# Kernel optimization log

Measured on AMD Instinct MI355X. Metric: run time of the kernel, lower is better.

## Reference

```python
import jax, jax.numpy as jnp
import numpy as np

N = 100000   # nodes
E = 1600000  # edges
F_IN = 32    # num_features
H = 16       # hidden_size (hardcoded as conv2 input in source)
C = 10       # num_classes
K = 2        # kernel_size (dim=1)


def setup_inputs() -> dict:
    key = jax.random.key(0)
    ks = jax.random.split(key, 9)
    x = jax.random.normal(ks[0], (N, F_IN), dtype=jnp.float32)
    edge_index = jax.random.randint(ks[1], (2, E), 0, N, dtype=jnp.int64)
    edge_attr = jax.random.uniform(ks[2], (E, 1), dtype=jnp.float32)
    s1 = 1.0 / np.sqrt(F_IN)
    s2 = 1.0 / np.sqrt(H)
    W1 = jax.random.normal(ks[3], (K, F_IN, H), dtype=jnp.float32) * s1
    root1 = jax.random.normal(ks[4], (F_IN, H), dtype=jnp.float32) * s1
    b1 = jnp.zeros((H,), dtype=jnp.float32)
    W2 = jax.random.normal(ks[5], (K, H, C), dtype=jnp.float32) * s2
    root2 = jax.random.normal(ks[6], (H, C), dtype=jnp.float32) * s2
    b2 = jnp.zeros((C,), dtype=jnp.float32)
    return {"x": x, "edge_index": edge_index, "edge_attr": edge_attr,
            "W1": W1, "root1": root1, "b1": b1,
            "W2": W2, "root2": root2, "b2": b2}


def spline_conv(x, edge_index, edge_attr, W, root, bias, num_nodes):
    # Open B-spline, degree 1: hat-function basis over K knots.
    k = W.shape[0]
    src, dst = edge_index[0], edge_index[1]
    v = edge_attr[:, 0] * (k - 1)                                   # [E]
    grid = jnp.arange(k, dtype=v.dtype)
    basis = jnp.maximum(0.0, 1.0 - jnp.abs(v[:, None] - grid[None, :]))  # [E,K]
    xe = x[src]                                                      # [E,in] gather
    msg = jnp.einsum('ei,kio,ek->eo', xe, W, basis)                  # per-edge message
    agg = jax.ops.segment_sum(msg, dst, num_segments=num_nodes)      # scatter-add
    deg = jax.ops.segment_sum(jnp.ones((msg.shape[0],), x.dtype), dst,
                              num_segments=num_nodes)
    agg = agg / jnp.maximum(deg, 1.0)[:, None]                       # mean aggregation
    return agg + x @ root + bias


def reference(x, edge_index, edge_attr, W1, root1, b1, W2, root2, b2):
    # Inference mode: F.dropout(training=False) is identity.
    h = jax.nn.elu(spline_conv(x, edge_index, edge_attr, W1, root1, b1, N))
    out = spline_conv(h, edge_index, edge_attr, W2, root2, b2, N)
    return jax.nn.log_softmax(out, axis=1)
```

## Files before the change

### kernel.cpp

```cpp
#include <hip/hip_runtime.h>
#include <math.h>

#define N_NODES 100000
#define E_EDGES 1600000
#define F_IN 32
#define HID 16
#define NC 10
#define SRC_BITS 17
#define SRC_MASK ((1u << SRC_BITS) - 1u)
#define VQ_SCALE 32767.0f
#define CBITS 9
#define BUCKET_N 512
#define NCB ((N_NODES + BUCKET_N - 1) / BUCKET_N)
#define BLK_E 8192
#define NBLK ((E_EDGES + BLK_E - 1) / BLK_E)
#define NODE_GRID ((N_NODES + 255) / 256)

__device__ __forceinline__ unsigned int bf16pair(float lo, float hi) {
    unsigned int ulo = __float_as_uint(lo), uhi = __float_as_uint(hi);
    ulo += 0x7fffu + ((ulo >> 16) & 1u);
    uhi += 0x7fffu + ((uhi >> 16) & 1u);
    return (ulo >> 16) | (uhi & 0xffff0000u);
}

__device__ __forceinline__ float lerp_pair(unsigned int pair, float v) {
    float a = __uint_as_float(pair << 16);
    float b = __uint_as_float(pair & 0xffff0000u);
    return fmaf(v, b - a, a);
}

__global__ __launch_bounds__(256) void fused_l1cnt(
    const float* __restrict__ x, const float* __restrict__ W1,
    const float* __restrict__ root1, const float* __restrict__ b1,
    const int* __restrict__ ei,
    unsigned int* __restrict__ y, float* __restrict__ r1,
    int* __restrict__ cnt)
{
    if (blockIdx.x >= NODE_GRID) {
        __shared__ int h[NCB];
        int b = blockIdx.x - NODE_GRID;
        for (int i = threadIdx.x; i < NCB; i += 256) h[i] = 0;
        __syncthreads();
        const int* dstp = ei + E_EDGES;
        int e0 = b * BLK_E;
        for (int i = threadIdx.x * 4; i < BLK_E; i += 1024) {
            int e = e0 + i;
            if (e + 3 < E_EDGES) {
                int4 d4 = *(const int4*)(dstp + e);
                atomicAdd(&h[d4.x >> CBITS], 1);
                atomicAdd(&h[d4.y >> CBITS], 1);
                atomicAdd(&h[d4.z >> CBITS], 1);
                atomicAdd(&h[d4.w >> CBITS], 1);
            } else {
                for (int k = 0; k < 4; k++)
                    if (e + k < E_EDGES) atomicAdd(&h[dstp[e + k] >> CBITS], 1);
            }
        }
        __syncthreads();
        for (int s = threadIdx.x; s < NCB; s += 256)
            cnt[s * NBLK + b] = h[s];
        return;
    }
    __shared__ float sW0[F_IN * HID], sW1[F_IN * HID], sR[F_IN * HID], sB[HID];
    for (int i = threadIdx.x; i < F_IN * HID; i += 256) {
        sW0[i] = W1[i];
        sW1[i] = W1[F_IN * HID + i];
        sR[i]  = root1[i];
    }
    if (threadIdx.x < HID) sB[threadIdx.x] = b1[threadIdx.x];
    __syncthreads();

    int n = blockIdx.x * 256 + threadIdx.x;
    if (n >= N_NODES) return;

    float xr[F_IN];
    const float4* xp = (const float4*)(x + (size_t)n * F_IN);
    #pragma unroll
    for (int i = 0; i < F_IN / 4; i++) {
        float4 t = xp[i];
        xr[i*4+0] = t.x; xr[i*4+1] = t.y; xr[i*4+2] = t.z; xr[i*4+3] = t.w;
    }

    float a0[HID], a1[HID], ar[HID];
    #pragma unroll
    for (int o = 0; o < HID; o++) { a0[o] = 0.f; a1[o] = 0.f; ar[o] = sB[o]; }
    for (int i = 0; i < F_IN; i++) {
        float xi = xr[i];
        #pragma unroll
        for (int o = 0; o < HID; o++) {
            a0[o] += xi * sW0[i * HID + o];
            a1[o] += xi * sW1[i * HID + o];
            ar[o] += xi * sR[i * HID + o];
        }
    }
    unsigned int* py = y + (size_t)n * 16;
    float* pr = r1 + (size_t)n * HID;
    #pragma unroll
    for (int o = 0; o < HID; o++) {
        py[o] = bf16pair(a0[o], a1[o]);
        pr[o] = ar[o];
    }
}

__global__ __launch_bounds__(256) void k_bucket(
    const int* __restrict__ ei, const float* __restrict__ ea,
    const int* __restrict__ cnt,
    int2* __restrict__ ebuf, int* __restrict__ bb, int* __restrict__ start)
{
    __shared__ int wsum[4], woff[4];
    __shared__ int base[NCB], cur[NCB];
    int t = threadIdx.x;
    int total = 0, myPref = 0;
    if (t < NCB) {
        const int* row = cnt + t * NBLK;
        int B = blockIdx.x;
        int s = 0;
        for (int b = 0; b < NBLK; b++) {
            if (b == B) myPref = s;
            s += row[b];
        }
        total = s;
    }
    int w = t >> 6, l = t & 63;
    int incl = total;
    #pragma unroll
    for (int off = 1; off < 64; off <<= 1) {
        int u = __shfl_up(incl, off, 64);
        if (l >= off) incl += u;
    }
    if (l == 63) wsum[w] = incl;
    __syncthreads();
    if (t == 0) {
        int a = 0;
        #pragma unroll
        for (int i = 0; i < 4; i++) { woff[i] = a; a += wsum[i]; }
    }
    __syncthreads();
    int excl = woff[w] + incl - total;
    if (t < NCB) {
        base[t] = excl + myPref;
        cur[t] = 0;
        if (blockIdx.x == 0) {
            bb[t] = excl;
            if (t == NCB - 1) { bb[NCB] = excl + total; start[N_NODES] = E_EDGES; }
        }
    }
    __syncthreads();

    const int* dstp = ei + E_EDGES;
    int e0 = blockIdx.x * BLK_E;
    for (int i = t * 4; i < BLK_E; i += 1024) {
        int e = e0 + i;
        if (e + 3 < E_EDGES) {
            int4 d4 = *(const int4*)(dstp + e);
            int4 s4 = *(const int4*)(ei + e);
            float4 a4 = *(const float4*)(ea + e);
            {
                int s = d4.x >> CBITS;
                int off = atomicAdd(&cur[s], 1);
                unsigned int vq = (unsigned int)(a4.x * VQ_SCALE + 0.5f);
                ebuf[base[s] + off] = make_int2(d4.x & (BUCKET_N - 1),
                                               (int)((vq << SRC_BITS) | (unsigned int)s4.x));
            }
            {
                int s = d4.y >> CBITS;
                int off = atomicAdd(&cur[s], 1);
                unsigned int vq = (unsigned int)(a4.y * VQ_SCALE + 0.5f);
                ebuf[base[s] + off] = make_int2(d4.y & (BUCKET_N - 1),
                                               (int)((vq << SRC_BITS) | (unsigned int)s4.y));
            }
            {
                int s = d4.z >> CBITS;
                int off = atomicAdd(&cur[s], 1);
                unsigned int vq = (unsigned int)(a4.z * VQ_SCALE + 0.5f);
                ebuf[base[s] + off] = make_int2(d4.z & (BUCKET_N - 1),
                                               (int)((vq << SRC_BITS) | (unsigned int)s4.z));
            }
            {
                int s = d4.w >> CBITS;
                int off = atomicAdd(&cur[s], 1);
                unsigned int vq = (unsigned int)(a4.w * VQ_SCALE + 0.5f);
                ebuf[base[s] + off] = make_int2(d4.w & (BUCKET_N - 1),
                                               (int)((vq << SRC_BITS) | (unsigned int)s4.w));
            }
        } else {
            for (int k = 0; k < 4; k++) {
                int ee = e + k;
                if (ee >= E_EDGES) break;
                int dst = dstp[ee];
                int s = dst >> CBITS;
                int off = atomicAdd(&cur[s], 1);
                unsigned int vq = (unsigned int)(ea[ee] * VQ_SCALE + 0.5f);
                ebuf[base[s] + off] = make_int2(dst & (BUCKET_N - 1),
                                               (int)((vq << SRC_BITS) | (unsigned int)ei[ee]));
            }
        }
    }
}

__global__ __launch_bounds__(512) void k_bsort(
    const int2* __restrict__ ebuf, const int* __restrict__ bb,
    unsigned int* __restrict__ es, int* __restrict__ start)
{
    __shared__ int hist[BUCKET_N];
    __shared__ int cursor[BUCKET_N];
    __shared__ int wsum[8], woff[8];
    int t = threadIdx.x;
    int b = blockIdx.x;
    int j0 = bb[b], j1 = bb[b + 1];
    hist[t] = 0; cursor[t] = 0;
    __syncthreads();
    for (int j = j0 + t; j < j1; j += 512)
        atomicAdd(&hist[ebuf[j].x], 1);
    __syncthreads();
    int c = hist[t];
    int w = t >> 6, l = t & 63;
    int incl = c;
    #pragma unroll
    for (int off = 1; off < 64; off <<= 1) {
        int u = __shfl_up(incl, off, 64);
        if (l >= off) incl += u;
    }
    if (l == 63) wsum[w] = incl;
    __syncthreads();
    if (t == 0) {
        int acc = 0;
        #pragma unroll
        for (int i = 0; i < 8; i++) { woff[i] = acc; acc += wsum[i]; }
    }
    __syncthreads();
    int excl = woff[w] + incl - c;
    hist[t] = excl;
    int node = (b << CBITS) + t;
    if (node < N_NODES) start[node] = j0 + excl;
    __syncthreads();
    for (int j = j0 + t; j < j1; j += 512) {
        int2 p = ebuf[j];
        int off = atomicAdd(&cursor[p.x], 1);
        es[j0 + hist[p.x] + off] = (unsigned int)p.y;
    }
}

__global__ __launch_bounds__(256) void k_agg1(
    const unsigned int* __restrict__ es, const int* __restrict__ start,
    const unsigned int* __restrict__ y, const float* __restrict__ r1,
    const float* __restrict__ W2, const float* __restrict__ root2,
    const float* __restrict__ b2,
    unsigned int* __restrict__ z, float* __restrict__ r2)
{
    __shared__ float sh[16 * 17];
    __shared__ float sW0[HID * NC], sW1[HID * NC], sRt[HID * NC], sB2[NC];
    int t = threadIdx.x;
    if (t < HID * NC) { sW0[t] = W2[t]; sW1[t] = W2[HID * NC + t]; sRt[t] = root2[t]; }
    if (t >= HID * NC && t < HID * NC + NC) sB2[t - HID * NC] = b2[t - HID * NC];

    int idx = blockIdx.x * 256 + t;
    int n = idx >> 4, o = idx & 15, g = t >> 4;
    if (n < N_NODES) {
        int j0 = start[n], j1 = start[n + 1];
        float acc0 = 0.f, acc1 = 0.f, acc2 = 0.f, acc3 = 0.f;
        int j = j0;
        for (; j + 7 < j1; j += 8) {
            unsigned int p0 = es[j],   p1 = es[j+1], p2 = es[j+2], p3 = es[j+3];
            unsigned int p4 = es[j+4], p5 = es[j+5], p6 = es[j+6], p7 = es[j+7];
            unsigned int q0 = y[(size_t)(p0 & SRC_MASK) * 16 + o];
            unsigned int q1 = y[(size_t)(p1 & SRC_MASK) * 16 + o];
            unsigned int q2 = y[(size_t)(p2 & SRC_MASK) * 16 + o];
            unsigned int q3 = y[(size_t)(p3 & SRC_MASK) * 16 + o];
            unsigned int q4 = y[(size_t)(p4 & SRC_MASK) * 16 + o];
            unsigned int q5 = y[(size_t)(p5 & SRC_MASK) * 16 + o];
            unsigned int q6 = y[(size_t)(p6 & SRC_MASK) * 16 + o];
            unsigned int q7 = y[(size_t)(p7 & SRC_MASK) * 16 + o];
            acc0 += lerp_pair(q0, (float)(p0 >> SRC_BITS) * (1.0f / VQ_SCALE));
            acc1 += lerp_pair(q1, (float)(p1 >> SRC_BITS) * (1.0f / VQ_SCALE));
            acc2 += lerp_pair(q2, (float)(p2 >> SRC_BITS) * (1.0f / VQ_SCALE));
            acc3 += lerp_pair(q3, (float)(p3 >> SRC_BITS) * (1.0f / VQ_SCALE));
            acc0 += lerp_pair(q4, (float)(p4 >> SRC_BITS) * (1.0f / VQ_SCALE));
            acc1 += lerp_pair(q5, (float)(p5 >> SRC_BITS) * (1.0f / VQ_SCALE));
            acc2 += lerp_pair(q6, (float)(p6 >> SRC_BITS) * (1.0f / VQ_SCALE));
            acc3 += lerp_pair(q7, (float)(p7 >> SRC_BITS) * (1.0f / VQ_SCALE));
        }
        for (; j + 3 < j1; j += 4) {
            unsigned int p0 = es[j], p1 = es[j+1], p2 = es[j+2], p3 = es[j+3];
            unsigned int q0 = y[(size_t)(p0 & SRC_MASK) * 16 + o];
            unsigned int q1 = y[(size_t)(p1 & SRC_MASK) * 16 + o];
            unsigned int q2 = y[(size_t)(p2 & SRC_MASK) * 16 + o];
            unsigned int q3 = y[(size_t)(p3 & SRC_MASK) * 16 + o];
            acc0 += lerp_pair(q0, (float)(p0 >> SRC_BITS) * (1.0f / VQ_SCALE));
            acc1 += lerp_pair(q1, (float)(p1 >> SRC_BITS) * (1.0f / VQ_SCALE));
            acc2 += lerp_pair(q2, (float)(p2 >> SRC_BITS) * (1.0f / VQ_SCALE));
            acc3 += lerp_pair(q3, (float)(p3 >> SRC_BITS) * (1.0f / VQ_SCALE));
        }
        for (; j < j1; j++) {
            unsigned int p = es[j];
            unsigned int q = y[(size_t)(p & SRC_MASK) * 16 + o];
            acc0 += lerp_pair(q, (float)(p >> SRC_BITS) * (1.0f / VQ_SCALE));
        }
        float acc = (acc0 + acc1) + (acc2 + acc3);
        float inv = 1.0f / fmaxf((float)(j1 - j0), 1.0f);
        float hv = acc * inv + r1[(size_t)n * HID + o];
        sh[g * 17 + o] = hv > 0.0f ? hv : expm1f(hv);
    }
    __syncthreads();

    int n2 = blockIdx.x * 16 + g;
    if (n2 < N_NODES) {
        int cc = o;
        unsigned int* pz = z + (size_t)n2 * 16;
        if (cc < NC) {
            float a0 = 0.f, a1 = 0.f, ar = sB2[cc];
            #pragma unroll
            for (int i = 0; i < HID; i++) {
                float hi = sh[g * 17 + i];
                a0 += hi * sW0[i * NC + cc];
                a1 += hi * sW1[i * NC + cc];
                ar += hi * sRt[i * NC + cc];
            }
            pz[cc] = bf16pair(a0, a1);
            r2[(size_t)n2 * NC + cc] = ar;
        } else {
            pz[cc] = 0u;
        }
    }
}

__global__ __launch_bounds__(256) void k_agg2(
    const unsigned int* __restrict__ es, const int* __restrict__ start,
    const unsigned int* __restrict__ z,
    const float* __restrict__ r2, float* __restrict__ out)
{
    int idx = blockIdx.x * 256 + threadIdx.x;
    int n = idx >> 4, o = idx & 15;
    if (n >= N_NODES) return;
    int j0 = start[n], j1 = start[n + 1];
    float acc0 = 0.f, acc1 = 0.f, acc2 = 0.f, acc3 = 0.f;
    int j = j0;
    for (; j + 7 < j1; j += 8) {
        unsigned int p0 = es[j],   p1 = es[j+1], p2 = es[j+2], p3 = es[j+3];
        unsigned int p4 = es[j+4], p5 = es[j+5], p6 = es[j+6], p7 = es[j+7];
        unsigned int q0 = z[(size_t)(p0 & SRC_MASK) * 16 + o];
        unsigned int q1 = z[(size_t)(p1 & SRC_MASK) * 16 + o];
        unsigned int q2 = z[(size_t)(p2 & SRC_MASK) * 16 + o];
        unsigned int q3 = z[(size_t)(p3 & SRC_MASK) * 16 + o];
        unsigned int q4 = z[(size_t)(p4 & SRC_MASK) * 16 + o];
        unsigned int q5 = z[(size_t)(p5 & SRC_MASK) * 16 + o];
        unsigned int q6 = z[(size_t)(p6 & SRC_MASK) * 16 + o];
        unsigned int q7 = z[(size_t)(p7 & SRC_MASK) * 16 + o];
        acc0 += lerp_pair(q0, (float)(p0 >> SRC_BITS) * (1.0f / VQ_SCALE));
        acc1 += lerp_pair(q1, (float)(p1 >> SRC_BITS) * (1.0f / VQ_SCALE));
        acc2 += lerp_pair(q2, (float)(p2 >> SRC_BITS) * (1.0f / VQ_SCALE));
        acc3 += lerp_pair(q3, (float)(p3 >> SRC_BITS) * (1.0f / VQ_SCALE));
        acc0 += lerp_pair(q4, (float)(p4 >> SRC_BITS) * (1.0f / VQ_SCALE));
        acc1 += lerp_pair(q5, (float)(p5 >> SRC_BITS) * (1.0f / VQ_SCALE));
        acc2 += lerp_pair(q6, (float)(p6 >> SRC_BITS) * (1.0f / VQ_SCALE));
        acc3 += lerp_pair(q7, (float)(p7 >> SRC_BITS) * (1.0f / VQ_SCALE));
    }
    for (; j + 3 < j1; j += 4) {
        unsigned int p0 = es[j], p1 = es[j+1], p2 = es[j+2], p3 = es[j+3];
        unsigned int q0 = z[(size_t)(p0 & SRC_MASK) * 16 + o];
        unsigned int q1 = z[(size_t)(p1 & SRC_MASK) * 16 + o];
        unsigned int q2 = z[(size_t)(p2 & SRC_MASK) * 16 + o];
        unsigned int q3 = z[(size_t)(p3 & SRC_MASK) * 16 + o];
        acc0 += lerp_pair(q0, (float)(p0 >> SRC_BITS) * (1.0f / VQ_SCALE));
        acc1 += lerp_pair(q1, (float)(p1 >> SRC_BITS) * (1.0f / VQ_SCALE));
        acc2 += lerp_pair(q2, (float)(p2 >> SRC_BITS) * (1.0f / VQ_SCALE));
        acc3 += lerp_pair(q3, (float)(p3 >> SRC_BITS) * (1.0f / VQ_SCALE));
    }
    for (; j < j1; j++) {
        unsigned int p = es[j];
        unsigned int q = z[(size_t)(p & SRC_MASK) * 16 + o];
        acc0 += lerp_pair(q, (float)(p >> SRC_BITS) * (1.0f / VQ_SCALE));
    }
    float acc = (acc0 + acc1) + (acc2 + acc3);
    float val = -INFINITY;
    if (o < NC) {
        float inv = 1.0f / fmaxf((float)(j1 - j0), 1.0f);
        val = acc * inv + r2[(size_t)n * NC + o];
    }
    float mx = val;
    #pragma unroll
    for (int off = 8; off > 0; off >>= 1) mx = fmaxf(mx, __shfl_xor(mx, off, 16));
    float ex = (o < NC) ? expf(val - mx) : 0.0f;
    float ssum = ex;
    #pragma unroll
    for (int off = 8; off > 0; off >>= 1) ssum += __shfl_xor(ssum, off, 16);
    if (o < NC) out[(size_t)n * NC + o] = val - mx - logf(ssum);
}

extern "C" void kernel_launch(void* const* d_in, const int* in_sizes, int n_in,
                              void* d_out, int out_size, void* d_ws, size_t ws_size,
                              hipStream_t stream) {
    const float* x     = (const float*)d_in[0];
    const int*   ei    = (const int*)d_in[1];
    const float* ea    = (const float*)d_in[2];
    const float* W1    = (const float*)d_in[3];
    const float* root1 = (const float*)d_in[4];
    const float* b1    = (const float*)d_in[5];
    const float* W2    = (const float*)d_in[6];
    const float* root2 = (const float*)d_in[7];
    const float* b2    = (const float*)d_in[8];
    float* out = (float*)d_out;

    char* wsb = (char*)d_ws;
    int2*         ebuf   = (int2*)wsb;
    unsigned int* es     = (unsigned int*)(wsb + (size_t)E_EDGES * 8);
    unsigned int* y      = es + (size_t)E_EDGES;
    float*        r1     = (float*)(y + (size_t)N_NODES * 16);
    unsigned int* z      = (unsigned int*)(r1 + (size_t)N_NODES * HID);
    float*        r2     = (float*)(z + (size_t)N_NODES * 16);
    int*          start  = (int*)(r2 + (size_t)N_NODES * NC);
    int*          cnt    = start + N_NODES + 1;
    int*          bb     = cnt + NCB * NBLK;

    int aggGrid  = (N_NODES * 16 + 255) / 256;

    fused_l1cnt<<<NODE_GRID + NBLK, 256, 0, stream>>>(x, W1, root1, b1, ei, y, r1, cnt);
    k_bucket<<<NBLK, 256, 0, stream>>>(ei, ea, cnt, ebuf, bb, start);
    k_bsort <<<NCB, 512, 0, stream>>>(ebuf, bb, es, start);
    k_agg1  <<<aggGrid, 256, 0, stream>>>(es, start, y, r1, W2, root2, b2, z, r2);
    k_agg2  <<<aggGrid, 256, 0, stream>>>(es, start, z, r2, out);
}
```

Before: 186.6 us.

## Shrink edge blocks and buckets, add separate row-scan kernel for bucket offsets

Edge blocks shrink from 8192 to 2048 edges and buckets from 512 to 256 nodes, so the bucket-scatter and per-bucket sort stages launch more, smaller blocks and spread across more compute units. A new k_rowscan kernel turns each bucket's per-block counts into exclusive prefix sums plus a per-bucket total. Before, every k_bucket thread serially walked a whole count row. k_bucket and k_bsort get wider thread blocks to match the new bucket counts. The trade-off is an extra kernel launch, a larger count matrix in memory, and more global atomics-free passes over it.

```diff
diff --git a/kernel.cpp b/kernel.cpp
--- a/kernel.cpp
+++ b/kernel.cpp
@@ -9,10 +9,10 @@
 #define SRC_BITS 17
 #define SRC_MASK ((1u << SRC_BITS) - 1u)
 #define VQ_SCALE 32767.0f
-#define CBITS 9
-#define BUCKET_N 512
+#define CBITS 8
+#define BUCKET_N 256
 #define NCB ((N_NODES + BUCKET_N - 1) / BUCKET_N)
-#define BLK_E 8192
+#define BLK_E 2048
 #define NBLK ((E_EDGES + BLK_E - 1) / BLK_E)
 #define NODE_GRID ((N_NODES + 255) / 256)
 
@@ -58,7 +58,7 @@
         }
         __syncthreads();
         for (int s = threadIdx.x; s < NCB; s += 256)
-            cnt[s * NBLK + b] = h[s];
+            cnt[(size_t)s * NBLK + b] = h[s];
         return;
     }
     __shared__ float sW0[F_IN * HID], sW1[F_IN * HID], sR[F_IN * HID], sB[HID];
@@ -102,27 +102,51 @@
     }
 }
 
-__global__ __launch_bounds__(256) void k_bucket(
+__global__ __launch_bounds__(256) void k_rowscan(
+    int* __restrict__ cnt, int* __restrict__ total)
+{
+    __shared__ int wsum[4], woff[4];
+    int s = blockIdx.x;
+    int t = threadIdx.x;
+    int w = t >> 6, l = t & 63;
+    int carry = 0;
+    int* row = cnt + (size_t)s * NBLK;
+    for (int c = 0; c < NBLK; c += 256) {
+        int idx = c + t;
+        int v = (idx < NBLK) ? row[idx] : 0;
+        int incl = v;
+        #pragma unroll
+        for (int off = 1; off < 64; off <<= 1) {
+            int u = __shfl_up(incl, off, 64);
+            if (l >= off) incl += u;
+        }
+        if (l == 63) wsum[w] = incl;
+        __syncthreads();
+        if (t == 0) {
+            int a = 0;
+            #pragma unroll
+            for (int i = 0; i < 4; i++) { woff[i] = a; a += wsum[i]; }
+        }
+        __syncthreads();
+        int excl = woff[w] + incl - v;
+        if (idx < NBLK) row[idx] = carry + excl;
+        carry += woff[3] + wsum[3];
+        __syncthreads();
+    }
+    if (t == 0) total[s] = carry;
+}
+
+__global__ __launch_bounds__(512) void k_bucket(
     const int* __restrict__ ei, const float* __restrict__ ea,
-    const int* __restrict__ cnt,
+    const int* __restrict__ cnt, const int* __restrict__ total,
     int2* __restrict__ ebuf, int* __restrict__ bb, int* __restrict__ start)
 {
-    __shared__ int wsum[4], woff[4];
+    __shared__ int wsum[8], woff[8];
     __shared__ int base[NCB], cur[NCB];
     int t = threadIdx.x;
-    int total = 0, myPref = 0;
-    if (t < NCB) {
-        const int* row = cnt + t * NBLK;
-        int B = blockIdx.x;
-        int s = 0;
-        for (int b = 0; b < NBLK; b++) {
-            if (b == B) myPref = s;
-            s += row[b];
-        }
-        total = s;
-    }
+    int tot = (t < NCB) ? total[t] : 0;
     int w = t >> 6, l = t & 63;
-    int incl = total;
+    int incl = tot;
     #pragma unroll
     for (int off = 1; off < 64; off <<= 1) {
         int u = __shfl_up(incl, off, 64);
@@ -133,23 +157,23 @@
     if (t == 0) {
         int a = 0;
         #pragma unroll
-        for (int i = 0; i < 4; i++) { woff[i] = a; a += wsum[i]; }
-    }
-    __syncthreads();
-    int excl = woff[w] + incl - total;
+        for (int i = 0; i < 8; i++) { woff[i] = a; a += wsum[i]; }
+    }
+    __syncthreads();
+    int excl = woff[w] + incl - tot;
     if (t < NCB) {
-        base[t] = excl + myPref;
+        base[t] = excl + cnt[(size_t)t * NBLK + blockIdx.x];
         cur[t] = 0;
         if (blockIdx.x == 0) {
             bb[t] = excl;
-            if (t == NCB - 1) { bb[NCB] = excl + total; start[N_NODES] = E_EDGES; }
+            if (t == NCB - 1) { bb[NCB] = excl + tot; start[N_NODES] = E_EDGES; }
         }
     }
     __syncthreads();
 
     const int* dstp = ei + E_EDGES;
     int e0 = blockIdx.x * BLK_E;
-    for (int i = t * 4; i < BLK_E; i += 1024) {
+    for (int i = t * 4; i < BLK_E; i += 2048) {
         int e = e0 + i;
         if (e + 3 < E_EDGES) {
             int4 d4 = *(const int4*)(dstp + e);
@@ -198,22 +222,22 @@
     }
 }
 
-__global__ __launch_bounds__(512) void k_bsort(
+__global__ __launch_bounds__(1024) void k_bsort(
     const int2* __restrict__ ebuf, const int* __restrict__ bb,
     unsigned int* __restrict__ es, int* __restrict__ start)
 {
     __shared__ int hist[BUCKET_N];
     __shared__ int cursor[BUCKET_N];
-    __shared__ int wsum[8], woff[8];
+    __shared__ int wsum[4], woff[4];
     int t = threadIdx.x;
     int b = blockIdx.x;
     int j0 = bb[b], j1 = bb[b + 1];
-    hist[t] = 0; cursor[t] = 0;
-    __syncthreads();
-    for (int j = j0 + t; j < j1; j += 512)
+    if (t < BUCKET_N) { hist[t] = 0; cursor[t] = 0; }
+    __syncthreads();
+    for (int j = j0 + t; j < j1; j += 1024)
         atomicAdd(&hist[ebuf[j].x], 1);
     __syncthreads();
-    int c = hist[t];
+    int c = (t < BUCKET_N) ? hist[t] : 0;
     int w = t >> 6, l = t & 63;
     int incl = c;
     #pragma unroll
@@ -221,20 +245,22 @@
         int u = __shfl_up(incl, off, 64);
         if (l >= off) incl += u;
     }
-    if (l == 63) wsum[w] = incl;
+    if (w < 4 && l == 63) wsum[w] = incl;
     __syncthreads();
     if (t == 0) {
         int acc = 0;
         #pragma unroll
-        for (int i = 0; i < 8; i++) { woff[i] = acc; acc += wsum[i]; }
-    }
-    __syncthreads();
-    int excl = woff[w] + incl - c;
-    hist[t] = excl;
-    int node = (b << CBITS) + t;
-    if (node < N_NODES) start[node] = j0 + excl;
-    __syncthreads();
-    for (int j = j0 + t; j < j1; j += 512) {
+        for (int i = 0; i < 4; i++) { woff[i] = acc; acc += wsum[i]; }
+    }
+    __syncthreads();
+    if (t < BUCKET_N) {
+        int excl = woff[w] + incl - c;
+        hist[t] = excl;
+        int node = (b << CBITS) + t;
+        if (node < N_NODES) start[node] = j0 + excl;
+    }
+    __syncthreads();
+    for (int j = j0 + t; j < j1; j += 1024) {
         int2 p = ebuf[j];
         int off = atomicAdd(&cursor[p.x], 1);
         es[j0 + hist[p.x] + off] = (unsigned int)p.y;
@@ -410,13 +436,15 @@
     float*        r2     = (float*)(z + (size_t)N_NODES * 16);
     int*          start  = (int*)(r2 + (size_t)N_NODES * NC);
     int*          cnt    = start + N_NODES + 1;
-    int*          bb     = cnt + NCB * NBLK;
+    int*          total  = cnt + (size_t)NCB * NBLK;
+    int*          bb     = total + NCB;
 
     int aggGrid  = (N_NODES * 16 + 255) / 256;
 
     fused_l1cnt<<<NODE_GRID + NBLK, 256, 0, stream>>>(x, W1, root1, b1, ei, y, r1, cnt);
-    k_bucket<<<NBLK, 256, 0, stream>>>(ei, ea, cnt, ebuf, bb, start);
-    k_bsort <<<NCB, 512, 0, stream>>>(ebuf, bb, es, start);
+    k_rowscan<<<NCB, 256, 0, stream>>>(cnt, total);
+    k_bucket<<<NBLK, 512, 0, stream>>>(ei, ea, cnt, total, ebuf, bb, start);
+    k_bsort <<<NCB, 1024, 0, stream>>>(ebuf, bb, es, start);
     k_agg1  <<<aggGrid, 256, 0, stream>>>(es, start, y, r1, W2, root2, b2, z, r2);
     k_agg2  <<<aggGrid, 256, 0, stream>>>(es, start, z, r2, out);
 }
```

Measured after the change: 185.5 us. No clear change (-0.6%).

## Replace two-pass bucket sort with global-atomic degree count, scan, and scatter CSR build

Applied to the files above, without the earlier changes.

Replaces the LDS-histogram bucket-then-local-sort CSR construction with a per-node degree count using global atomics, a two-level prefix scan, and a direct scatter that claims slots with global atomics on per-node cursors. This drops the intermediate 8-byte ebuf pass and the bucket-sort kernel. In exchange it depends on contended global atomics (1.6M per pass, twice), does random 4-byte writes into es, adds a memset and two scan launches, and makes edge order within each node nondeterministic.

```diff
diff --git a/kernel.cpp b/kernel.cpp
--- a/kernel.cpp
+++ b/kernel.cpp
@@ -9,12 +9,11 @@
 #define SRC_BITS 17
 #define SRC_MASK ((1u << SRC_BITS) - 1u)
 #define VQ_SCALE 32767.0f
-#define CBITS 9
-#define BUCKET_N 512
-#define NCB ((N_NODES + BUCKET_N - 1) / BUCKET_N)
-#define BLK_E 8192
-#define NBLK ((E_EDGES + BLK_E - 1) / BLK_E)
+#define DBLK_E 4096
+#define NDBLK ((E_EDGES + DBLK_E - 1) / DBLK_E)
 #define NODE_GRID ((N_NODES + 255) / 256)
+#define SCAN_BLK 512
+#define NSCAN ((N_NODES + SCAN_BLK - 1) / SCAN_BLK)
 
 __device__ __forceinline__ unsigned int bf16pair(float lo, float hi) {
     unsigned int ulo = __float_as_uint(lo), uhi = __float_as_uint(hi);
@@ -29,36 +28,30 @@
     return fmaf(v, b - a, a);
 }
 
-__global__ __launch_bounds__(256) void fused_l1cnt(
+__global__ __launch_bounds__(256) void fused_l1deg(
     const float* __restrict__ x, const float* __restrict__ W1,
     const float* __restrict__ root1, const float* __restrict__ b1,
     const int* __restrict__ ei,
     unsigned int* __restrict__ y, float* __restrict__ r1,
-    int* __restrict__ cnt)
+    int* __restrict__ deg)
 {
     if (blockIdx.x >= NODE_GRID) {
-        __shared__ int h[NCB];
         int b = blockIdx.x - NODE_GRID;
-        for (int i = threadIdx.x; i < NCB; i += 256) h[i] = 0;
-        __syncthreads();
         const int* dstp = ei + E_EDGES;
-        int e0 = b * BLK_E;
-        for (int i = threadIdx.x * 4; i < BLK_E; i += 1024) {
+        int e0 = b * DBLK_E;
+        for (int i = threadIdx.x * 4; i < DBLK_E; i += 1024) {
             int e = e0 + i;
             if (e + 3 < E_EDGES) {
                 int4 d4 = *(const int4*)(dstp + e);
-                atomicAdd(&h[d4.x >> CBITS], 1);
-                atomicAdd(&h[d4.y >> CBITS], 1);
-                atomicAdd(&h[d4.z >> CBITS], 1);
-                atomicAdd(&h[d4.w >> CBITS], 1);
+                atomicAdd(&deg[d4.x], 1);
+                atomicAdd(&deg[d4.y], 1);
+                atomicAdd(&deg[d4.z], 1);
+                atomicAdd(&deg[d4.w], 1);
             } else {
                 for (int k = 0; k < 4; k++)
-                    if (e + k < E_EDGES) atomicAdd(&h[dstp[e + k] >> CBITS], 1);
+                    if (e + k < E_EDGES) atomicAdd(&deg[dstp[e + k]], 1);
             }
         }
-        __syncthreads();
-        for (int s = threadIdx.x; s < NCB; s += 256)
-            cnt[s * NBLK + b] = h[s];
         return;
     }
     __shared__ float sW0[F_IN * HID], sW1[F_IN * HID], sR[F_IN * HID], sB[HID];
@@ -102,33 +95,48 @@
     }
 }
 
-__global__ __launch_bounds__(256) void k_bucket(
-    const int* __restrict__ ei, const float* __restrict__ ea,
-    const int* __restrict__ cnt,
-    int2* __restrict__ ebuf, int* __restrict__ bb, int* __restrict__ start)
-{
-    __shared__ int wsum[4], woff[4];
-    __shared__ int base[NCB], cur[NCB];
+__global__ __launch_bounds__(512) void k_scan1(
+    const int* __restrict__ deg, int* __restrict__ start, int* __restrict__ part)
+{
+    __shared__ int wsum[8], woff[8];
     int t = threadIdx.x;
-    int total = 0, myPref = 0;
-    if (t < NCB) {
-        const int* row = cnt + t * NBLK;
-        int B = blockIdx.x;
-        int s = 0;
-        for (int b = 0; b < NBLK; b++) {
-            if (b == B) myPref = s;
-            s += row[b];
-        }
-        total = s;
-    }
+    int node = blockIdx.x * SCAN_BLK + t;
+    int v = (node < N_NODES) ? deg[node] : 0;
     int w = t >> 6, l = t & 63;
-    int incl = total;
+    int incl = v;
     #pragma unroll
     for (int off = 1; off < 64; off <<= 1) {
         int u = __shfl_up(incl, off, 64);
         if (l >= off) incl += u;
     }
     if (l == 63) wsum[w] = incl;
+    __syncthreads();
+    if (t == 0) {
+        int a = 0;
+        #pragma unroll
+        for (int i = 0; i < 8; i++) { woff[i] = a; a += wsum[i]; }
+        part[blockIdx.x] = a;
+    }
+    __syncthreads();
+    int excl = woff[w] + incl - v;
+    if (node < N_NODES) start[node] = excl;
+}
+
+__global__ __launch_bounds__(512) void k_scan2(
+    const int* __restrict__ part, int* __restrict__ start, int* __restrict__ cursor)
+{
+    __shared__ int wsum[4], woff[4];
+    __shared__ int sE[NSCAN];
+    int t = threadIdx.x;
+    int v = (t < NSCAN) ? part[t] : 0;
+    int w = t >> 6, l = t & 63;
+    int incl = v;
+    #pragma unroll
+    for (int off = 1; off < 64; off <<= 1) {
+        int u = __shfl_up(incl, off, 64);
+        if (l >= off) incl += u;
+    }
+    if (w < 4 && l == 63) wsum[w] = incl;
     __syncthreads();
     if (t == 0) {
         int a = 0;
@@ -136,108 +144,57 @@
         for (int i = 0; i < 4; i++) { woff[i] = a; a += wsum[i]; }
     }
     __syncthreads();
-    int excl = woff[w] + incl - total;
-    if (t < NCB) {
-        base[t] = excl + myPref;
-        cur[t] = 0;
-        if (blockIdx.x == 0) {
-            bb[t] = excl;
-            if (t == NCB - 1) { bb[NCB] = excl + total; start[N_NODES] = E_EDGES; }
-        }
-    }
-    __syncthreads();
-
+    if (t < NSCAN) sE[t] = woff[w] + incl - v;
+    __syncthreads();
+    int base = sE[blockIdx.x];
+    int node = blockIdx.x * SCAN_BLK + t;
+    if (node < N_NODES) {
+        int s = start[node] + base;
+        start[node] = s;
+        cursor[node] = s;
+    }
+    if (blockIdx.x == 0 && t == 0) start[N_NODES] = E_EDGES;
+}
+
+__global__ __launch_bounds__(512) void k_scatter(
+    const int* __restrict__ ei, const float* __restrict__ ea,
+    int* __restrict__ cursor, unsigned int* __restrict__ es)
+{
+    int i = (blockIdx.x * 512 + threadIdx.x) * 4;
+    if (i >= E_EDGES) return;
     const int* dstp = ei + E_EDGES;
-    int e0 = blockIdx.x * BLK_E;
-    for (int i = t * 4; i < BLK_E; i += 1024) {
-        int e = e0 + i;
-        if (e + 3 < E_EDGES) {
-            int4 d4 = *(const int4*)(dstp + e);
-            int4 s4 = *(const int4*)(ei + e);
-            float4 a4 = *(const float4*)(ea + e);
-            {
-                int s = d4.x >> CBITS;
-                int off = atomicAdd(&cur[s], 1);
-                unsigned int vq = (unsigned int)(a4.x * VQ_SCALE + 0.5f);
-                ebuf[base[s] + off] = make_int2(d4.x & (BUCKET_N - 1),
-                                               (int)((vq << SRC_BITS) | (unsigned int)s4.x));
-            }
-            {
-                int s = d4.y >> CBITS;
-                int off = atomicAdd(&cur[s], 1);
-                unsigned int vq = (unsigned int)(a4.y * VQ_SCALE + 0.5f);
-                ebuf[base[s] + off] = make_int2(d4.y & (BUCKET_N - 1),
-                                               (int)((vq << SRC_BITS) | (unsigned int)s4.y));
-            }
-            {
-                int s = d4.z >> CBITS;
-                int off = atomicAdd(&cur[s], 1);
-                unsigned int vq = (unsigned int)(a4.z * VQ_SCALE + 0.5f);
-                ebuf[base[s] + off] = make_int2(d4.z & (BUCKET_N - 1),
-                                               (int)((vq << SRC_BITS) | (unsigned int)s4.z));
-            }
-            {
-                int s = d4.w >> CBITS;
-                int off = atomicAdd(&cur[s], 1);
-                unsigned int vq = (unsigned int)(a4.w * VQ_SCALE + 0.5f);
-                ebuf[base[s] + off] = make_int2(d4.w & (BUCKET_N - 1),
-                                               (int)((vq << SRC_BITS) | (unsigned int)s4.w));
-            }
-        } else {
-            for (int k = 0; k < 4; k++) {
-                int ee = e + k;
-                if (ee >= E_EDGES) break;
-                int dst = dstp[ee];
-                int s = dst >> CBITS;
-                int off = atomicAdd(&cur[s], 1);
-                unsigned int vq = (unsigned int)(ea[ee] * VQ_SCALE + 0.5f);
-                ebuf[base[s] + off] = make_int2(dst & (BUCKET_N - 1),
-                                               (int)((vq << SRC_BITS) | (unsigned int)ei[ee]));
-            }
-        }
-    }
-}
-
-__global__ __launch_bounds__(512) void k_bsort(
-    const int2* __restrict__ ebuf, const int* __restrict__ bb,
-    unsigned int* __restrict__ es, int* __restrict__ start)
-{
-    __shared__ int hist[BUCKET_N];
-    __shared__ int cursor[BUCKET_N];
-    __shared__ int wsum[8], woff[8];
-    int t = threadIdx.x;
-    int b = blockIdx.x;
-    int j0 = bb[b], j1 = bb[b + 1];
-    hist[t] = 0; cursor[t] = 0;
-    __syncthreads();
-    for (int j = j0 + t; j < j1; j += 512)
-        atomicAdd(&hist[ebuf[j].x], 1);
-    __syncthreads();
-    int c = hist[t];
-    int w = t >> 6, l = t & 63;
-    int incl = c;
-    #pragma unroll
-    for (int off = 1; off < 64; off <<= 1) {
-        int u = __shfl_up(incl, off, 64);
-        if (l >= off) incl += u;
-    }
-    if (l == 63) wsum[w] = incl;
-    __syncthreads();
-    if (t == 0) {
-        int acc = 0;
-        #pragma unroll
-        for (int i = 0; i < 8; i++) { woff[i] = acc; acc += wsum[i]; }
-    }
-    __syncthreads();
-    int excl = woff[w] + incl - c;
-    hist[t] = excl;
-    int node = (b << CBITS) + t;
-    if (node < N_NODES) start[node] = j0 + excl;
-    __syncthreads();
-    for (int j = j0 + t; j < j1; j += 512) {
-        int2 p = ebuf[j];
-        int off = atomicAdd(&cursor[p.x], 1);
-        es[j0 + hist[p.x] + off] = (unsigned int)p.y;
+    if (i + 3 < E_EDGES) {
+        int4 s4 = *(const int4*)(ei + i);
+        int4 d4 = *(const int4*)(dstp + i);
+        float4 a4 = *(const float4*)(ea + i);
+        {
+            int idx = atomicAdd(&cursor[d4.x], 1);
+            unsigned int vq = (unsigned int)(a4.x * VQ_SCALE + 0.5f);
+            es[idx] = (vq << SRC_BITS) | (unsigned int)s4.x;
+        }
+        {
+            int idx = atomicAdd(&cursor[d4.y], 1);
+            unsigned int vq = (unsigned int)(a4.y * VQ_SCALE + 0.5f);
+            es[idx] = (vq << SRC_BITS) | (unsigned int)s4.y;
+        }
+        {
+            int idx = atomicAdd(&cursor[d4.z], 1);
+            unsigned int vq = (unsigned int)(a4.z * VQ_SCALE + 0.5f);
+            es[idx] = (vq << SRC_BITS) | (unsigned int)s4.z;
+        }
+        {
+            int idx = atomicAdd(&cursor[d4.w], 1);
+            unsigned int vq = (unsigned int)(a4.w * VQ_SCALE + 0.5f);
+            es[idx] = (vq << SRC_BITS) | (unsigned int)s4.w;
+        }
+    } else {
+        for (int k = 0; k < 4; k++) {
+            int e = i + k;
+            if (e >= E_EDGES) break;
+            int idx = atomicAdd(&cursor[dstp[e]], 1);
+            unsigned int vq = (unsigned int)(ea[e] * VQ_SCALE + 0.5f);
+            es[idx] = (vq << SRC_BITS) | (unsigned int)ei[e];
+        }
     }
 }
 
@@ -402,21 +359,24 @@
     float* out = (float*)d_out;
 
     char* wsb = (char*)d_ws;
-    int2*         ebuf   = (int2*)wsb;
-    unsigned int* es     = (unsigned int*)(wsb + (size_t)E_EDGES * 8);
+    unsigned int* es     = (unsigned int*)wsb;
     unsigned int* y      = es + (size_t)E_EDGES;
     float*        r1     = (float*)(y + (size_t)N_NODES * 16);
     unsigned int* z      = (unsigned int*)(r1 + (size_t)N_NODES * HID);
     float*        r2     = (float*)(z + (size_t)N_NODES * 16);
     int*          start  = (int*)(r2 + (size_t)N_NODES * NC);
-    int*          cnt    = start + N_NODES + 1;
-    int*          bb     = cnt + NCB * NBLK;
+    int*          cursor = start + N_NODES + 1;
+    int*          deg    = cursor + N_NODES;
+    int*          part   = deg + N_NODES;
 
     int aggGrid  = (N_NODES * 16 + 255) / 256;
-
-    fused_l1cnt<<<NODE_GRID + NBLK, 256, 0, stream>>>(x, W1, root1, b1, ei, y, r1, cnt);
-    k_bucket<<<NBLK, 256, 0, stream>>>(ei, ea, cnt, ebuf, bb, start);
-    k_bsort <<<NCB, 512, 0, stream>>>(ebuf, bb, es, start);
+    int scatGrid = (E_EDGES / 4 + 511) / 512;
+
+    hipMemsetAsync(deg, 0, (size_t)N_NODES * sizeof(int), stream);
+    fused_l1deg<<<NODE_GRID + NDBLK, 256, 0, stream>>>(x, W1, root1, b1, ei, y, r1, deg);
+    k_scan1 <<<NSCAN, SCAN_BLK, 0, stream>>>(deg, start, part);
+    k_scan2 <<<NSCAN, SCAN_BLK, 0, stream>>>(part, start, cursor);
+    k_scatter<<<scatGrid, 512, 0, stream>>>(ei, ea, cursor, es);
     k_agg1  <<<aggGrid, 256, 0, stream>>>(es, start, y, r1, W2, root2, b2, z, r2);
     k_agg2  <<<aggGrid, 256, 0, stream>>>(es, start, z, r2, out);
 }
```

Measured after the change: 341.8 us. +83.2%, slower.

## Fuse bucket sort with layer-1 aggregation and halve bucket size

Applied to the files above, without the earlier changes.

Merges the per-bucket counting sort with the first-layer aggregation and dense transform into one kernel. Each block sorts its bucket's edges in LDS, then aggregates those nodes using LDS-held offsets and degrees, and shares each node's hidden vector across 16 lanes with shuffles instead of shared memory. Bucket width drops from 512 to 256 nodes, so the bucket kernel moves to 512 threads to cover the larger bucket count. This removes one launch and the reread of start offsets, but runs layer-1 aggregation on only ~391 blocks, which may expose gather latency.

```diff
diff --git a/kernel.cpp b/kernel.cpp
--- a/kernel.cpp
+++ b/kernel.cpp
@@ -9,8 +9,8 @@
 #define SRC_BITS 17
 #define SRC_MASK ((1u << SRC_BITS) - 1u)
 #define VQ_SCALE 32767.0f
-#define CBITS 9
-#define BUCKET_N 512
+#define CBITS 8
+#define BUCKET_N 256
 #define NCB ((N_NODES + BUCKET_N - 1) / BUCKET_N)
 #define BLK_E 8192
 #define NBLK ((E_EDGES + BLK_E - 1) / BLK_E)
@@ -58,7 +58,7 @@
         }
         __syncthreads();
         for (int s = threadIdx.x; s < NCB; s += 256)
-            cnt[s * NBLK + b] = h[s];
+            cnt[(size_t)s * NBLK + b] = h[s];
         return;
     }
     __shared__ float sW0[F_IN * HID], sW1[F_IN * HID], sR[F_IN * HID], sB[HID];
@@ -102,17 +102,17 @@
     }
 }
 
-__global__ __launch_bounds__(256) void k_bucket(
+__global__ __launch_bounds__(512) void k_bucket(
     const int* __restrict__ ei, const float* __restrict__ ea,
     const int* __restrict__ cnt,
     int2* __restrict__ ebuf, int* __restrict__ bb, int* __restrict__ start)
 {
-    __shared__ int wsum[4], woff[4];
+    __shared__ int wsum[8], woff[8];
     __shared__ int base[NCB], cur[NCB];
     int t = threadIdx.x;
     int total = 0, myPref = 0;
     if (t < NCB) {
-        const int* row = cnt + t * NBLK;
+        const int* row = cnt + (size_t)t * NBLK;
         int B = blockIdx.x;
         int s = 0;
         for (int b = 0; b < NBLK; b++) {
@@ -133,7 +133,7 @@
     if (t == 0) {
         int a = 0;
         #pragma unroll
-        for (int i = 0; i < 4; i++) { woff[i] = a; a += wsum[i]; }
+        for (int i = 0; i < 8; i++) { woff[i] = a; a += wsum[i]; }
     }
     __syncthreads();
     int excl = woff[w] + incl - total;
@@ -149,7 +149,7 @@
 
     const int* dstp = ei + E_EDGES;
     int e0 = blockIdx.x * BLK_E;
-    for (int i = t * 4; i < BLK_E; i += 1024) {
+    for (int i = t * 4; i < BLK_E; i += 2048) {
         int e = e0 + i;
         if (e + 3 < E_EDGES) {
             int4 d4 = *(const int4*)(dstp + e);
@@ -198,22 +198,32 @@
     }
 }
 
-__global__ __launch_bounds__(512) void k_bsort(
+__global__ __launch_bounds__(512) void k_bsort_agg1(
     const int2* __restrict__ ebuf, const int* __restrict__ bb,
-    unsigned int* __restrict__ es, int* __restrict__ start)
+    const unsigned int* __restrict__ y, const float* __restrict__ r1,
+    const float* __restrict__ W2, const float* __restrict__ root2,
+    const float* __restrict__ b2,
+    unsigned int* __restrict__ es, int* __restrict__ start,
+    unsigned int* __restrict__ z, float* __restrict__ r2)
 {
     __shared__ int hist[BUCKET_N];
     __shared__ int cursor[BUCKET_N];
+    __shared__ int sdeg[BUCKET_N];
     __shared__ int wsum[8], woff[8];
+    __shared__ float sW0[HID * NC], sW1[HID * NC], sRt[HID * NC], sB2[NC];
     int t = threadIdx.x;
     int b = blockIdx.x;
     int j0 = bb[b], j1 = bb[b + 1];
-    hist[t] = 0; cursor[t] = 0;
-    __syncthreads();
+    if (t < BUCKET_N) { hist[t] = 0; cursor[t] = 0; }
+    if (t < HID * NC) { sW0[t] = W2[t]; sW1[t] = W2[HID * NC + t]; sRt[t] = root2[t]; }
+    if (t >= HID * NC && t < HID * NC + NC) sB2[t - HID * NC] = b2[t - HID * NC];
+    __syncthreads();
+
     for (int j = j0 + t; j < j1; j += 512)
         atomicAdd(&hist[ebuf[j].x], 1);
     __syncthreads();
-    int c = hist[t];
+
+    int c = (t < BUCKET_N) ? hist[t] : 0;
     int w = t >> 6, l = t & 63;
     int incl = c;
     #pragma unroll
@@ -226,41 +236,35 @@
     if (t == 0) {
         int acc = 0;
         #pragma unroll
-        for (int i = 0; i < 8; i++) { woff[i] = acc; acc += wsum[i]; }
-    }
-    __syncthreads();
-    int excl = woff[w] + incl - c;
-    hist[t] = excl;
-    int node = (b << CBITS) + t;
-    if (node < N_NODES) start[node] = j0 + excl;
-    __syncthreads();
+        for (int i = 0; i < 4; i++) { woff[i] = acc; acc += wsum[i]; }
+    }
+    __syncthreads();
+    if (t < BUCKET_N) {
+        int excl = woff[w] + incl - c;
+        sdeg[t] = c;
+        hist[t] = excl;
+        int node = (b << CBITS) + t;
+        if (node < N_NODES) start[node] = j0 + excl;
+    }
+    __syncthreads();
+
     for (int j = j0 + t; j < j1; j += 512) {
         int2 p = ebuf[j];
         int off = atomicAdd(&cursor[p.x], 1);
         es[j0 + hist[p.x] + off] = (unsigned int)p.y;
     }
-}
-
-__global__ __launch_bounds__(256) void k_agg1(
-    const unsigned int* __restrict__ es, const int* __restrict__ start,
-    const unsigned int* __restrict__ y, const float* __restrict__ r1,
-    const float* __restrict__ W2, const float* __restrict__ root2,
-    const float* __restrict__ b2,
-    unsigned int* __restrict__ z, float* __restrict__ r2)
-{
-    __shared__ float sh[16 * 17];
-    __shared__ float sW0[HID * NC], sW1[HID * NC], sRt[HID * NC], sB2[NC];
-    int t = threadIdx.x;
-    if (t < HID * NC) { sW0[t] = W2[t]; sW1[t] = W2[HID * NC + t]; sRt[t] = root2[t]; }
-    if (t >= HID * NC && t < HID * NC + NC) sB2[t - HID * NC] = b2[t - HID * NC];
-
-    int idx = blockIdx.x * 256 + t;
-    int n = idx >> 4, o = idx & 15, g = t >> 4;
-    if (n < N_NODES) {
-        int j0 = start[n], j1 = start[n + 1];
+    __syncthreads();
+
+    int o = t & 15, g = t >> 4;
+    for (int n = g; n < BUCKET_N; n += 32) {
+        int node = (b << CBITS) + n;
+        if (node >= N_NODES) break;
+        int jj0 = j0 + hist[n];
+        int deg = sdeg[n];
+        int jj1 = jj0 + deg;
         float acc0 = 0.f, acc1 = 0.f, acc2 = 0.f, acc3 = 0.f;
-        int j = j0;
-        for (; j + 7 < j1; j += 8) {
+        int j = jj0;
+        for (; j + 7 < jj1; j += 8) {
             unsigned int p0 = es[j],   p1 = es[j+1], p2 = es[j+2], p3 = es[j+3];
             unsigned int p4 = es[j+4], p5 = es[j+5], p6 = es[j+6], p7 = es[j+7];
             unsigned int q0 = y[(size_t)(p0 & SRC_MASK) * 16 + o];
@@ -280,7 +284,7 @@
             acc2 += lerp_pair(q6, (float)(p6 >> SRC_BITS) * (1.0f / VQ_SCALE));
             acc3 += lerp_pair(q7, (float)(p7 >> SRC_BITS) * (1.0f / VQ_SCALE));
         }
-        for (; j + 3 < j1; j += 4) {
+        for (; j + 3 < jj1; j += 4) {
             unsigned int p0 = es[j], p1 = es[j+1], p2 = es[j+2], p3 = es[j+3];
             unsigned int q0 = y[(size_t)(p0 & SRC_MASK) * 16 + o];
             unsigned int q1 = y[(size_t)(p1 & SRC_MASK) * 16 + o];
@@ -291,35 +295,32 @@
             acc2 += lerp_pair(q2, (float)(p2 >> SRC_BITS) * (1.0f / VQ_SCALE));
             acc3 += lerp_pair(q3, (float)(p3 >> SRC_BITS) * (1.0f / VQ_SCALE));
         }
-        for (; j < j1; j++) {
+        for (; j < jj1; j++) {
             unsigned int p = es[j];
             unsigned int q = y[(size_t)(p & SRC_MASK) * 16 + o];
             acc0 += lerp_pair(q, (float)(p >> SRC_BITS) * (1.0f / VQ_SCALE));
         }
         float acc = (acc0 + acc1) + (acc2 + acc3);
-        float inv = 1.0f / fmaxf((float)(j1 - j0), 1.0f);
-        float hv = acc * inv + r1[(size_t)n * HID + o];
-        sh[g * 17 + o] = hv > 0.0f ? hv : expm1f(hv);
-    }
-    __syncthreads();
-
-    int n2 = blockIdx.x * 16 + g;
-    if (n2 < N_NODES) {
-        int cc = o;
-        unsigned int* pz = z + (size_t)n2 * 16;
-        if (cc < NC) {
-            float a0 = 0.f, a1 = 0.f, ar = sB2[cc];
-            #pragma unroll
-            for (int i = 0; i < HID; i++) {
-                float hi = sh[g * 17 + i];
-                a0 += hi * sW0[i * NC + cc];
-                a1 += hi * sW1[i * NC + cc];
-                ar += hi * sRt[i * NC + cc];
-            }
-            pz[cc] = bf16pair(a0, a1);
-            r2[(size_t)n2 * NC + cc] = ar;
+        float inv = 1.0f / fmaxf((float)deg, 1.0f);
+        float hv = acc * inv + r1[(size_t)node * HID + o];
+        hv = hv > 0.0f ? hv : expm1f(hv);
+
+        float a0 = 0.f, a1 = 0.f, ar = (o < NC) ? sB2[o] : 0.f;
+        #pragma unroll
+        for (int i = 0; i < HID; i++) {
+            float hi = __shfl(hv, i, 16);
+            if (o < NC) {
+                a0 += hi * sW0[i * NC + o];
+                a1 += hi * sW1[i * NC + o];
+                ar += hi * sRt[i * NC + o];
+            }
+        }
+        unsigned int* pz = z + (size_t)node * 16;
+        if (o < NC) {
+            pz[o] = bf16pair(a0, a1);
+            r2[(size_t)node * NC + o] = ar;
         } else {
-            pz[cc] = 0u;
+            pz[o] = 0u;
         }
     }
 }
@@ -410,13 +411,12 @@
     float*        r2     = (float*)(z + (size_t)N_NODES * 16);
     int*          start  = (int*)(r2 + (size_t)N_NODES * NC);
     int*          cnt    = start + N_NODES + 1;
-    int*          bb     = cnt + NCB * NBLK;
-
-    int aggGrid  = (N_NODES * 16 + 255) / 256;
-
-    fused_l1cnt<<<NODE_GRID + NBLK, 256, 0, stream>>>(x, W1, root1, b1, ei, y, r1, cnt);
-    k_bucket<<<NBLK, 256, 0, stream>>>(ei, ea, cnt, ebuf, bb, start);
-    k_bsort <<<NCB, 512, 0, stream>>>(ebuf, bb, es, start);
-    k_agg1  <<<aggGrid, 256, 0, stream>>>(es, start, y, r1, W2, root2, b2, z, r2);
-    k_agg2  <<<aggGrid, 256, 0, stream>>>(es, start, z, r2, out);
-}
+    int*          bb     = cnt + (size_t)NCB * NBLK;
+
+    int aggGrid = (N_NODES * 16 + 255) / 256;
+
+    fused_l1cnt <<<NODE_GRID + NBLK, 256, 0, stream>>>(x, W1, root1, b1, ei, y, r1, cnt);
+    k_bucket    <<<NBLK, 512, 0, stream>>>(ei, ea, cnt, ebuf, bb, start);
+    k_bsort_agg1<<<NCB, 512, 0, stream>>>(ebuf, bb, y, r1, W2, root2, b2, es, start, z, r2);
+    k_agg2      <<<aggGrid, 256, 0, stream>>>(es, start, z, r2, out);
+}
```

New measurement: 208.3 us. 11.6% more time.
